# Kernel tuning notes

Hardware: AMD Instinct MI355X
Metric: run time of the kernel (lower is better)

## Reference

```python
import jax, jax.numpy as jnp
import numpy as np

N_NODES = 50000
N_EDGES = 640000
D = 128


def setup_inputs() -> dict:
    key = jax.random.key(0)
    k1, k2, k3, k4, k5 = jax.random.split(key, 5)
    graph_embedding = jax.random.normal(k1, (N_NODES, D), dtype=jnp.float32)
    # xavier_uniform for a (1, D) tensor: bound = sqrt(6/(1+D))
    bound = float(np.sqrt(6.0 / (1 + D)))
    weight = jax.random.uniform(k2, (1, D), dtype=jnp.float32, minval=-bound, maxval=bound)
    e_feat = jax.random.randint(k3, (N_EDGES,), 0, 31, dtype=jnp.int64)
    src = jax.random.randint(k4, (N_EDGES,), 0, N_NODES, dtype=jnp.int64)
    dst = jax.random.randint(k5, (N_EDGES,), 0, N_NODES, dtype=jnp.int64)
    return {"graph_embedding": graph_embedding, "weight": weight,
            "e_feat": e_feat, "src": src, "dst": dst}


def reference(graph_embedding, weight, e_feat, src, dst):
    n_nodes = graph_embedding.shape[0]
    # emb == ft == ft0 == ft1 == ft2 == ft3 in the original module
    emb = jax.nn.elu(graph_embedding * weight)  # [N, D]
    e = e_feat.reshape(-1, 1).astype(jnp.float32)  # [E, 1] (module casts to float)
    # res + sum_k where(e==type_k, ft_k, 0) with all ft_k identical ->
    # per-edge multiplier 1 + matched-type indicators
    mult = (1.0
            + (e == 0.0).astype(emb.dtype)
            + (e == 6.0).astype(emb.dtype)
            + (e == 14.0).astype(emb.dtype)
            + (e == 30.0).astype(emb.dtype))  # [E, 1]
    msgs = emb[src] * mult  # [E, D] gather + mask-select
    # fn.sum('m','ft'): scatter-add messages to destination nodes
    return jax.ops.segment_sum(msgs, dst, num_segments=n_nodes)  # [N, D]
```

## Files before the change

### kernel.cpp

```cpp
#include <hip/hip_runtime.h>

#define D        128
#define NT       256
#define NBMAX    256
#define CAPB     8192
#define KA_BLKS  320
#define OVF_CAP  65536

typedef __attribute__((ext_vector_type(4))) _Float16 half4;
typedef __attribute__((ext_vector_type(4))) float    f32x4;

__device__ __forceinline__ float4 elu_mul(float4 g, float4 w) {
    float4 v;
    v.x = g.x * w.x; v.y = g.y * w.y; v.z = g.z * w.z; v.w = g.w * w.w;
    v.x = (v.x > 0.0f) ? v.x : (__expf(v.x) - 1.0f);
    v.y = (v.y > 0.0f) ? v.y : (__expf(v.y) - 1.0f);
    v.z = (v.z > 0.0f) ? v.z : (__expf(v.z) - 1.0f);
    v.w = (v.w > 0.0f) ? v.w : (__expf(v.w) - 1.0f);
    return v;
}

__global__ __launch_bounds__(NT)
void emb_kernel(const float* __restrict__ ge, const float* __restrict__ weight,
                _Float16* __restrict__ emb, int* __restrict__ cursor,
                int* __restrict__ ovf_cnt, int n_nodes, int nbins) {
    int t = blockIdx.x * NT + threadIdx.x;
    if (t < nbins) cursor[t] = t * CAPB;
    if (t == 0) *ovf_cnt = 0;

    int quads = n_nodes * (D / 4);
    if (t < quads) {
        int col = (t & 31) * 4;
        float4 g = *reinterpret_cast<const float4*>(ge + (size_t)t * 4);
        float4 w = *reinterpret_cast<const float4*>(weight + col);
        float4 v = elu_mul(g, w);
        half4 h;
        h.x = (_Float16)v.x; h.y = (_Float16)v.y;
        h.z = (_Float16)v.z; h.w = (_Float16)v.w;
        *reinterpret_cast<half4*>(emb + (size_t)t * 4) = h;
    }
}

__global__ __launch_bounds__(NT)
void bin_kernel(const int* __restrict__ e_feat, const int* __restrict__ src,
                const int* __restrict__ dst, int* __restrict__ cursor,
                uint2* __restrict__ binned, int* __restrict__ ovf_cnt,
                uint2* __restrict__ ovf, int n_edges, int nbins, int per_block) {
    __shared__ int hist[NBMAX];
    __shared__ int base[NBMAX];
    __shared__ int rk[NBMAX];
    int t = threadIdx.x;
    for (int i = t; i < NBMAX; i += NT) { hist[i] = 0; rk[i] = 0; }
    __syncthreads();

    int e0 = blockIdx.x * per_block;
    int e1 = e0 + per_block; if (e1 > n_edges) e1 = n_edges;

    for (int e = e0 + t; e < e1; e += NT)
        atomicAdd(&hist[dst[e] >> 8], 1);
    __syncthreads();

    for (int b = t; b < nbins; b += NT)
        base[b] = hist[b] ? atomicAdd(&cursor[b], hist[b]) : 0;
    __syncthreads();

    for (int e = e0 + t; e < e1; e += NT) {
        int d = dst[e];
        int b = d >> 8;
        int f = e_feat[e];
        unsigned int flag = (f == 0 || f == 6 || f == 14 || f == 30) ? 1u : 0u;
        unsigned int rec  = (unsigned int)src[e] | (flag << 31);
        int r = atomicAdd(&rk[b], 1);
        long long pos = (long long)base[b] + r;
        if (pos < (long long)(b + 1) * CAPB) {
            binned[pos] = make_uint2(rec, (unsigned int)(d & 255));
        } else {
            int op = atomicAdd(ovf_cnt, 1);
            if (op < OVF_CAP) ovf[op] = make_uint2(rec, (unsigned int)d);
        }
    }
}

__global__ __launch_bounds__(1024)
void csr_kernel(const uint2* __restrict__ binned, const int* __restrict__ cursor,
                int* __restrict__ offsets, unsigned int* __restrict__ bucket,
                int n_nodes, int nbins) {
    __shared__ int s[NBMAX];
    __shared__ int cnt2[NBMAX];
    __shared__ int off2[NBMAX];
    __shared__ int rk2[NBMAX];
    int t = threadIdx.x;
    int b = blockIdx.x;

    int c = 0;
    if (t < nbins) {
        int raw = cursor[t] - t * CAPB;
        c = raw < CAPB ? raw : CAPB;
    }
    if (t < NBMAX) s[t] = c;
    __syncthreads();
    for (int d = 1; d < NBMAX; d <<= 1) {
        int x = 0;
        if (t < NBMAX && t >= d) x = s[t - d];
        __syncthreads();
        if (t < NBMAX) s[t] += x;
        __syncthreads();
    }
    int rawb = cursor[b] - b * CAPB;
    int cntb = rawb < CAPB ? rawb : CAPB;
    int G = s[b] - cntb;
    int total = s[nbins - 1];

    for (int i = t; i < NBMAX; i += 1024) { cnt2[i] = 0; rk2[i] = 0; }
    __syncthreads();
    const uint2* rb = binned + (long long)b * CAPB;
    for (int i = t; i < cntb; i += 1024)
        atomicAdd(&cnt2[rb[i].y], 1);
    __syncthreads();
    if (t < NBMAX) off2[t] = cnt2[t];
    __syncthreads();
    for (int d = 1; d < NBMAX; d <<= 1) {
        int x = 0;
        if (t < NBMAX && t >= d) x = off2[t - d];
        __syncthreads();
        if (t < NBMAX) off2[t] += x;
        __syncthreads();
    }

    int base_node = b << 8;
    if (t < NBMAX) {
        int node = base_node + t;
        if (node <= n_nodes) offsets[node] = G + off2[t] - cnt2[t];
    }
    if (b == nbins - 1 && t == 0) offsets[n_nodes] = total;
    __syncthreads();

    for (int i = t; i < cntb; i += 1024) {
        uint2 r = rb[i];
        int l = (int)r.y;
        int p = atomicAdd(&rk2[l], 1);
        bucket[G + (off2[l] - cnt2[l]) + p] = r.x;
    }
}

__global__ __launch_bounds__(NT)
void gather_kernel(const _Float16* __restrict__ emb,
                   const int* __restrict__ offsets,
                   const unsigned int* __restrict__ bucket,
                   const int* __restrict__ ovf_cnt, const uint2* __restrict__ ovf,
                   float* __restrict__ out, int n_nodes) {
    int tid = blockIdx.x * NT + threadIdx.x;
    int node = tid >> 5;
    if (node >= n_nodes) return;
    int col = (tid & 31) * 4;

    int beg = offsets[node];
    int end = offsets[node + 1];
    float4 acc = make_float4(0.f, 0.f, 0.f, 0.f);

    int i = beg;
    for (; i + 8 <= end; i += 8) {
        unsigned int r0 = bucket[i+0], r1 = bucket[i+1], r2 = bucket[i+2], r3 = bucket[i+3];
        unsigned int r4 = bucket[i+4], r5 = bucket[i+5], r6 = bucket[i+6], r7 = bucket[i+7];
        half4 h0 = *reinterpret_cast<const half4*>(emb + (size_t)(r0 & 0x7FFFFFFFu) * D + col);
        half4 h1 = *reinterpret_cast<const half4*>(emb + (size_t)(r1 & 0x7FFFFFFFu) * D + col);
        half4 h2 = *reinterpret_cast<const half4*>(emb + (size_t)(r2 & 0x7FFFFFFFu) * D + col);
        half4 h3 = *reinterpret_cast<const half4*>(emb + (size_t)(r3 & 0x7FFFFFFFu) * D + col);
        half4 h4 = *reinterpret_cast<const half4*>(emb + (size_t)(r4 & 0x7FFFFFFFu) * D + col);
        half4 h5 = *reinterpret_cast<const half4*>(emb + (size_t)(r5 & 0x7FFFFFFFu) * D + col);
        half4 h6 = *reinterpret_cast<const half4*>(emb + (size_t)(r6 & 0x7FFFFFFFu) * D + col);
        half4 h7 = *reinterpret_cast<const half4*>(emb + (size_t)(r7 & 0x7FFFFFFFu) * D + col);
        float m0 = (r0 >> 31) ? 2.f : 1.f, m1 = (r1 >> 31) ? 2.f : 1.f;
        float m2 = (r2 >> 31) ? 2.f : 1.f, m3 = (r3 >> 31) ? 2.f : 1.f;
        float m4 = (r4 >> 31) ? 2.f : 1.f, m5 = (r5 >> 31) ? 2.f : 1.f;
        float m6 = (r6 >> 31) ? 2.f : 1.f, m7 = (r7 >> 31) ? 2.f : 1.f;
        acc.x += (float)h0.x*m0 + (float)h1.x*m1 + (float)h2.x*m2 + (float)h3.x*m3
               + (float)h4.x*m4 + (float)h5.x*m5 + (float)h6.x*m6 + (float)h7.x*m7;
        acc.y += (float)h0.y*m0 + (float)h1.y*m1 + (float)h2.y*m2 + (float)h3.y*m3
               + (float)h4.y*m4 + (float)h5.y*m5 + (float)h6.y*m6 + (float)h7.y*m7;
        acc.z += (float)h0.z*m0 + (float)h1.z*m1 + (float)h2.z*m2 + (float)h3.z*m3
               + (float)h4.z*m4 + (float)h5.z*m5 + (float)h6.z*m6 + (float)h7.z*m7;
        acc.w += (float)h0.w*m0 + (float)h1.w*m1 + (float)h2.w*m2 + (float)h3.w*m3
               + (float)h4.w*m4 + (float)h5.w*m5 + (float)h6.w*m6 + (float)h7.w*m7;
    }
    for (; i + 4 <= end; i += 4) {
        unsigned int r0 = bucket[i+0], r1 = bucket[i+1], r2 = bucket[i+2], r3 = bucket[i+3];
        half4 h0 = *reinterpret_cast<const half4*>(emb + (size_t)(r0 & 0x7FFFFFFFu) * D + col);
        half4 h1 = *reinterpret_cast<const half4*>(emb + (size_t)(r1 & 0x7FFFFFFFu) * D + col);
        half4 h2 = *reinterpret_cast<const half4*>(emb + (size_t)(r2 & 0x7FFFFFFFu) * D + col);
        half4 h3 = *reinterpret_cast<const half4*>(emb + (size_t)(r3 & 0x7FFFFFFFu) * D + col);
        float m0 = (r0 >> 31) ? 2.f : 1.f, m1 = (r1 >> 31) ? 2.f : 1.f;
        float m2 = (r2 >> 31) ? 2.f : 1.f, m3 = (r3 >> 31) ? 2.f : 1.f;
        acc.x += (float)h0.x*m0 + (float)h1.x*m1 + (float)h2.x*m2 + (float)h3.x*m3;
        acc.y += (float)h0.y*m0 + (float)h1.y*m1 + (float)h2.y*m2 + (float)h3.y*m3;
        acc.z += (float)h0.z*m0 + (float)h1.z*m1 + (float)h2.z*m2 + (float)h3.z*m3;
        acc.w += (float)h0.w*m0 + (float)h1.w*m1 + (float)h2.w*m2 + (float)h3.w*m3;
    }
    for (; i < end; ++i) {
        unsigned int r = bucket[i];
        half4 h = *reinterpret_cast<const half4*>(emb + (size_t)(r & 0x7FFFFFFFu) * D + col);
        float m = (r >> 31) ? 2.f : 1.f;
        acc.x += (float)h.x*m; acc.y += (float)h.y*m;
        acc.z += (float)h.z*m; acc.w += (float)h.w*m;
    }

    int no = *ovf_cnt;
    if (no > 0) {
        if (no > OVF_CAP) no = OVF_CAP;
        for (int k = 0; k < no; ++k) {
            uint2 o = ovf[k];
            if ((int)o.y == node) {
                half4 h = *reinterpret_cast<const half4*>(emb + (size_t)(o.x & 0x7FFFFFFFu) * D + col);
                float m = (o.x >> 31) ? 2.f : 1.f;
                acc.x += (float)h.x*m; acc.y += (float)h.y*m;
                acc.z += (float)h.z*m; acc.w += (float)h.w*m;
            }
        }
    }

    f32x4 o;
    o.x = acc.x; o.y = acc.y; o.z = acc.z; o.w = acc.w;
    __builtin_nontemporal_store(o, reinterpret_cast<f32x4*>(out + (size_t)node * D + col));
}

__global__ void edge_scatter_fallback(const float* __restrict__ ge,
                                      const float* __restrict__ weight,
                                      const int* __restrict__ e_feat,
                                      const int* __restrict__ src,
                                      const int* __restrict__ dst,
                                      float* __restrict__ out, int n_edges) {
    long long tid = (long long)blockIdx.x * blockDim.x + threadIdx.x;
    int edge = (int)(tid >> 5);
    if (edge >= n_edges) return;
    int col = (int)(tid & 31) * 4;
    int e = e_feat[edge];
    float mult = (e == 0 || e == 6 || e == 14 || e == 30) ? 2.0f : 1.0f;
    float4 w = *reinterpret_cast<const float4*>(weight + col);
    float4 g = *reinterpret_cast<const float4*>(ge + (long long)src[edge] * D + col);
    float4 v = elu_mul(g, w);
    float* o = out + (long long)dst[edge] * D + col;
    atomicAdd(o + 0, v.x * mult);
    atomicAdd(o + 1, v.y * mult);
    atomicAdd(o + 2, v.z * mult);
    atomicAdd(o + 3, v.w * mult);
}

extern "C" void kernel_launch(void* const* d_in, const int* in_sizes, int n_in,
                              void* d_out, int out_size, void* d_ws, size_t ws_size,
                              hipStream_t stream) {
    const float* ge     = (const float*)d_in[0];
    const float* weight = (const float*)d_in[1];
    const int*   e_feat = (const int*)d_in[2];
    const int*   src    = (const int*)d_in[3];
    const int*   dst    = (const int*)d_in[4];
    float* out = (float*)d_out;

    int n_edges = in_sizes[2];
    int n_nodes = out_size / D;
    int nbins   = (n_nodes + 255) >> 8;

    auto align256 = [](size_t x) { return (x + 255) & ~(size_t)255; };
    size_t o_emb    = 0;
    size_t o_cursor = o_emb    + align256((size_t)n_nodes * D * sizeof(_Float16));
    size_t o_ovfcnt = o_cursor + align256((size_t)NBMAX * 4);
    size_t o_offs   = o_ovfcnt + 256;
    size_t o_binned = o_offs   + align256((size_t)(n_nodes + 1) * 4);
    size_t o_bucket = o_binned + align256((size_t)NBMAX * CAPB * 8);
    size_t o_ovf    = o_bucket + align256((size_t)n_edges * 4);
    size_t need     = o_ovf + (size_t)OVF_CAP * 8 + 256;

    bool ok = (nbins <= NBMAX) && ((long long)n_edges <= (long long)nbins * CAPB);

    if (ws_size < need || !ok) {
        (void)hipMemsetAsync(d_out, 0, (size_t)out_size * sizeof(float), stream);
        long long total = (long long)n_edges * 32;
        edge_scatter_fallback<<<(int)((total + 255) / 256), 256, 0, stream>>>(
            ge, weight, e_feat, src, dst, out, n_edges);
        return;
    }

    char* ws = (char*)d_ws;
    _Float16*     emb     = (_Float16*)(ws + o_emb);
    int*          cursor  = (int*)(ws + o_cursor);
    int*          ovf_cnt = (int*)(ws + o_ovfcnt);
    int*          offsets = (int*)(ws + o_offs);
    uint2*        binned  = (uint2*)(ws + o_binned);
    unsigned int* bucket  = (unsigned int*)(ws + o_bucket);
    uint2*        ovf     = (uint2*)(ws + o_ovf);

    int quads = n_nodes * (D / 4);
    int k1b = (quads + NT - 1) / NT;
    int per_block = (n_edges + KA_BLKS - 1) / KA_BLKS;

    emb_kernel<<<k1b, NT, 0, stream>>>(ge, weight, emb, cursor, ovf_cnt,
                                       n_nodes, nbins);
    bin_kernel<<<KA_BLKS, NT, 0, stream>>>(e_feat, src, dst, cursor, binned,
                                           ovf_cnt, ovf, n_edges, nbins, per_block);
    csr_kernel<<<nbins, 1024, 0, stream>>>(binned, cursor, offsets, bucket,
                                           n_nodes, nbins);

    long long total = (long long)n_nodes * 32;
    gather_kernel<<<(int)((total + 255) / 256), NT, 0, stream>>>(
        emb, offsets, bucket, ovf_cnt, ovf, out, n_nodes);
}
```

Before: 63.54 us.

## Fuse binning with embedding and use per-block bin cells instead of global cursors

The embedding ELU/fp16 conversion and edge binning now run in one launch, with blocks split between the two roles. Binning writes into fixed per-(block,bin) cells of 64 entries, so the global histogram pass and the atomic cursor reservation are gone. The CSR kernel reads each bin's cells from all 320 blocks with one thread per cell. It writes (offset, degree) pairs into fixed-stride bucket regions, so no global prefix scan is needed. The cost is serial per-thread cell loops in csr_kernel, a larger workspace, and a spill path for cells that overflow.

```diff
diff --git a/kernel.cpp b/kernel.cpp
--- a/kernel.cpp
+++ b/kernel.cpp
@@ -1,11 +1,10 @@
 #include <hip/hip_runtime.h>
 
-#define D        128
-#define NT       256
-#define NBMAX    256
-#define CAPB     8192
-#define KA_BLKS  320
-#define OVF_CAP  65536
+#define D      128
+#define NT     256
+#define KB     320
+#define CAPBB  64
+#define NBMAX  256
 
 typedef __attribute__((ext_vector_type(4))) _Float16 half4;
 typedef __attribute__((ext_vector_type(4))) float    f32x4;
@@ -21,141 +20,137 @@
 }
 
 __global__ __launch_bounds__(NT)
-void emb_kernel(const float* __restrict__ ge, const float* __restrict__ weight,
-                _Float16* __restrict__ emb, int* __restrict__ cursor,
-                int* __restrict__ ovf_cnt, int n_nodes, int nbins) {
-    int t = blockIdx.x * NT + threadIdx.x;
-    if (t < nbins) cursor[t] = t * CAPB;
-    if (t == 0) *ovf_cnt = 0;
-
-    int quads = n_nodes * (D / 4);
-    if (t < quads) {
-        int col = (t & 31) * 4;
-        float4 g = *reinterpret_cast<const float4*>(ge + (size_t)t * 4);
-        float4 w = *reinterpret_cast<const float4*>(weight + col);
-        float4 v = elu_mul(g, w);
-        half4 h;
-        h.x = (_Float16)v.x; h.y = (_Float16)v.y;
-        h.z = (_Float16)v.z; h.w = (_Float16)v.w;
-        *reinterpret_cast<half4*>(emb + (size_t)t * 4) = h;
-    }
-}
-
-__global__ __launch_bounds__(NT)
-void bin_kernel(const int* __restrict__ e_feat, const int* __restrict__ src,
-                const int* __restrict__ dst, int* __restrict__ cursor,
-                uint2* __restrict__ binned, int* __restrict__ ovf_cnt,
-                uint2* __restrict__ ovf, int n_edges, int nbins, int per_block) {
-    __shared__ int hist[NBMAX];
-    __shared__ int base[NBMAX];
-    __shared__ int rk[NBMAX];
-    int t = threadIdx.x;
-    for (int i = t; i < NBMAX; i += NT) { hist[i] = 0; rk[i] = 0; }
-    __syncthreads();
-
-    int e0 = blockIdx.x * per_block;
-    int e1 = e0 + per_block; if (e1 > n_edges) e1 = n_edges;
-
-    for (int e = e0 + t; e < e1; e += NT)
-        atomicAdd(&hist[dst[e] >> 8], 1);
-    __syncthreads();
-
-    for (int b = t; b < nbins; b += NT)
-        base[b] = hist[b] ? atomicAdd(&cursor[b], hist[b]) : 0;
-    __syncthreads();
-
-    for (int e = e0 + t; e < e1; e += NT) {
-        int d = dst[e];
-        int b = d >> 8;
-        int f = e_feat[e];
-        unsigned int flag = (f == 0 || f == 6 || f == 14 || f == 30) ? 1u : 0u;
-        unsigned int rec  = (unsigned int)src[e] | (flag << 31);
-        int r = atomicAdd(&rk[b], 1);
-        long long pos = (long long)base[b] + r;
-        if (pos < (long long)(b + 1) * CAPB) {
-            binned[pos] = make_uint2(rec, (unsigned int)(d & 255));
-        } else {
-            int op = atomicAdd(ovf_cnt, 1);
-            if (op < OVF_CAP) ovf[op] = make_uint2(rec, (unsigned int)d);
+void fused_kernel(const float* __restrict__ ge, const float* __restrict__ weight,
+                  const int* __restrict__ e_feat, const int* __restrict__ src,
+                  const int* __restrict__ dst,
+                  _Float16* __restrict__ emb, uint2* __restrict__ binned,
+                  int* __restrict__ cnts, uint2* __restrict__ spill,
+                  int* __restrict__ spill_cnt,
+                  int n_nodes, int n_edges, int nbins, int per_block) {
+    if ((int)blockIdx.x < KB) {
+        __shared__ int rk[NBMAX];
+        __shared__ int sp;
+        int t = threadIdx.x;
+        for (int i = t; i < NBMAX; i += NT) rk[i] = 0;
+        if (t == 0) sp = 0;
+        __syncthreads();
+
+        int blk = blockIdx.x;
+        int e0 = blk * per_block;
+        int e1 = e0 + per_block; if (e1 > n_edges) e1 = n_edges;
+        for (int e = e0 + t; e < e1; e += NT) {
+            int d = dst[e];
+            int b = d >> 8;
+            int f = e_feat[e];
+            unsigned int flag = (f == 0 || f == 6 || f == 14 || f == 30) ? 1u : 0u;
+            unsigned int rec  = (unsigned int)src[e] | (flag << 31);
+            int r = atomicAdd(&rk[b], 1);
+            if (r < CAPBB) {
+                binned[((size_t)blk * nbins + b) * CAPBB + r] =
+                    make_uint2(rec, (unsigned int)(d & 255));
+            } else {
+                int s = atomicAdd(&sp, 1);
+                spill[(size_t)blk * per_block + s] = make_uint2(rec, (unsigned int)d);
+            }
         }
+        __syncthreads();
+        for (int b = t; b < nbins; b += NT)
+            cnts[blk * nbins + b] = rk[b] < CAPBB ? rk[b] : CAPBB;
+        if (t == 0) spill_cnt[blk] = sp;
+    } else {
+        int t = ((int)blockIdx.x - KB) * NT + threadIdx.x;
+        int quads = n_nodes * (D / 4);
+        if (t < quads) {
+            int col = (t & 31) * 4;
+            float4 g = *reinterpret_cast<const float4*>(ge + (size_t)t * 4);
+            float4 w = *reinterpret_cast<const float4*>(weight + col);
+            float4 v = elu_mul(g, w);
+            half4 h;
+            h.x = (_Float16)v.x; h.y = (_Float16)v.y;
+            h.z = (_Float16)v.z; h.w = (_Float16)v.w;
+            *reinterpret_cast<half4*>(emb + (size_t)t * 4) = h;
+        }
     }
 }
 
 __global__ __launch_bounds__(1024)
-void csr_kernel(const uint2* __restrict__ binned, const int* __restrict__ cursor,
-                int* __restrict__ offsets, unsigned int* __restrict__ bucket,
-                int n_nodes, int nbins) {
-    __shared__ int s[NBMAX];
+void csr_kernel(const uint2* __restrict__ binned, const int* __restrict__ cnts,
+                uint2* __restrict__ offdeg, unsigned int* __restrict__ bucket,
+                const int* __restrict__ spill_cnt, int* __restrict__ spill_total,
+                int n_nodes, int nbins, int capb_out) {
     __shared__ int cnt2[NBMAX];
     __shared__ int off2[NBMAX];
     __shared__ int rk2[NBMAX];
+    __shared__ int cellc[KB];
+    __shared__ int stot;
     int t = threadIdx.x;
     int b = blockIdx.x;
 
-    int c = 0;
-    if (t < nbins) {
-        int raw = cursor[t] - t * CAPB;
-        c = raw < CAPB ? raw : CAPB;
-    }
-    if (t < NBMAX) s[t] = c;
+    for (int i = t; i < NBMAX; i += 1024) { cnt2[i] = 0; rk2[i] = 0; }
+    if (t < KB) cellc[t] = cnts[t * nbins + b];
+    if (t == 0) stot = 0;
     __syncthreads();
-    for (int d = 1; d < NBMAX; d <<= 1) {
-        int x = 0;
-        if (t < NBMAX && t >= d) x = s[t - d];
-        __syncthreads();
-        if (t < NBMAX) s[t] += x;
-        __syncthreads();
-    }
-    int rawb = cursor[b] - b * CAPB;
-    int cntb = rawb < CAPB ? rawb : CAPB;
-    int G = s[b] - cntb;
-    int total = s[nbins - 1];
-
-    for (int i = t; i < NBMAX; i += 1024) { cnt2[i] = 0; rk2[i] = 0; }
+
+    if (t < KB) {
+        const uint2* cell = binned + ((size_t)t * nbins + b) * CAPBB;
+        int c = cellc[t];
+        for (int j = 0; j < c; ++j) atomicAdd(&cnt2[cell[j].y], 1);
+    }
     __syncthreads();
-    const uint2* rb = binned + (long long)b * CAPB;
-    for (int i = t; i < cntb; i += 1024)
-        atomicAdd(&cnt2[rb[i].y], 1);
-    __syncthreads();
+
     if (t < NBMAX) off2[t] = cnt2[t];
     __syncthreads();
-    for (int d = 1; d < NBMAX; d <<= 1) {
+    for (int d2 = 1; d2 < NBMAX; d2 <<= 1) {
         int x = 0;
-        if (t < NBMAX && t >= d) x = off2[t - d];
+        if (t < NBMAX && t >= d2) x = off2[t - d2];
         __syncthreads();
         if (t < NBMAX) off2[t] += x;
         __syncthreads();
     }
 
-    int base_node = b << 8;
+    int G = b * capb_out;
     if (t < NBMAX) {
-        int node = base_node + t;
-        if (node <= n_nodes) offsets[node] = G + off2[t] - cnt2[t];
-    }
-    if (b == nbins - 1 && t == 0) offsets[n_nodes] = total;
+        int node = (b << 8) + t;
+        if (node < n_nodes)
+            offdeg[node] = make_uint2((unsigned int)(G + off2[t] - cnt2[t]),
+                                      (unsigned int)cnt2[t]);
+    }
     __syncthreads();
 
-    for (int i = t; i < cntb; i += 1024) {
-        uint2 r = rb[i];
-        int l = (int)r.y;
-        int p = atomicAdd(&rk2[l], 1);
-        bucket[G + (off2[l] - cnt2[l]) + p] = r.x;
+    if (t < KB) {
+        const uint2* cell = binned + ((size_t)t * nbins + b) * CAPBB;
+        int c = cellc[t];
+        for (int j = 0; j < c; ++j) {
+            uint2 r = cell[j];
+            int l = (int)r.y;
+            int p = atomicAdd(&rk2[l], 1);
+            bucket[G + (off2[l] - cnt2[l]) + p] = r.x;
+        }
+    }
+
+    if (b == 0) {
+        if (t < KB && spill_cnt[t] > 0) atomicAdd(&stot, spill_cnt[t]);
+        __syncthreads();
+        if (t == 0) *spill_total = stot;
     }
 }
 
 __global__ __launch_bounds__(NT)
 void gather_kernel(const _Float16* __restrict__ emb,
-                   const int* __restrict__ offsets,
+                   const uint2* __restrict__ offdeg,
                    const unsigned int* __restrict__ bucket,
-                   const int* __restrict__ ovf_cnt, const uint2* __restrict__ ovf,
-                   float* __restrict__ out, int n_nodes) {
+                   const int* __restrict__ spill_total,
+                   const int* __restrict__ spill_cnt,
+                   const uint2* __restrict__ spill,
+                   float* __restrict__ out, int n_nodes, int per_block) {
     int tid = blockIdx.x * NT + threadIdx.x;
     int node = tid >> 5;
     if (node >= n_nodes) return;
     int col = (tid & 31) * 4;
 
-    int beg = offsets[node];
-    int end = offsets[node + 1];
+    uint2 od = offdeg[node];
+    int beg = (int)od.x;
+    int end = beg + (int)od.y;
     float4 acc = make_float4(0.f, 0.f, 0.f, 0.f);
 
     int i = beg;
@@ -204,16 +199,17 @@
         acc.z += (float)h.z*m; acc.w += (float)h.w*m;
     }
 
-    int no = *ovf_cnt;
-    if (no > 0) {
-        if (no > OVF_CAP) no = OVF_CAP;
-        for (int k = 0; k < no; ++k) {
-            uint2 o = ovf[k];
-            if ((int)o.y == node) {
-                half4 h = *reinterpret_cast<const half4*>(emb + (size_t)(o.x & 0x7FFFFFFFu) * D + col);
-                float m = (o.x >> 31) ? 2.f : 1.f;
-                acc.x += (float)h.x*m; acc.y += (float)h.y*m;
-                acc.z += (float)h.z*m; acc.w += (float)h.w*m;
+    if (*spill_total > 0) {
+        for (int blk = 0; blk < KB; ++blk) {
+            int sc = spill_cnt[blk];
+            for (int j = 0; j < sc; ++j) {
+                uint2 o = spill[(size_t)blk * per_block + j];
+                if ((int)o.y == node) {
+                    half4 h = *reinterpret_cast<const half4*>(emb + (size_t)(o.x & 0x7FFFFFFFu) * D + col);
+                    float m = (o.x >> 31) ? 2.f : 1.f;
+                    acc.x += (float)h.x*m; acc.y += (float)h.y*m;
+                    acc.z += (float)h.z*m; acc.w += (float)h.w*m;
+                }
             }
         }
     }
@@ -258,20 +254,21 @@
     int n_edges = in_sizes[2];
     int n_nodes = out_size / D;
     int nbins   = (n_nodes + 255) >> 8;
+    int per_block = (n_edges + KB - 1) / KB;
+    int capb_out  = KB * CAPBB;
 
     auto align256 = [](size_t x) { return (x + 255) & ~(size_t)255; };
     size_t o_emb    = 0;
-    size_t o_cursor = o_emb    + align256((size_t)n_nodes * D * sizeof(_Float16));
-    size_t o_ovfcnt = o_cursor + align256((size_t)NBMAX * 4);
-    size_t o_offs   = o_ovfcnt + 256;
-    size_t o_binned = o_offs   + align256((size_t)(n_nodes + 1) * 4);
-    size_t o_bucket = o_binned + align256((size_t)NBMAX * CAPB * 8);
-    size_t o_ovf    = o_bucket + align256((size_t)n_edges * 4);
-    size_t need     = o_ovf + (size_t)OVF_CAP * 8 + 256;
-
-    bool ok = (nbins <= NBMAX) && ((long long)n_edges <= (long long)nbins * CAPB);
-
-    if (ws_size < need || !ok) {
+    size_t o_binned = o_emb    + align256((size_t)n_nodes * D * sizeof(_Float16));
+    size_t o_spill  = o_binned + align256((size_t)KB * nbins * CAPBB * 8);
+    size_t o_cnts   = o_spill  + align256((size_t)KB * per_block * 8);
+    size_t o_scnt   = o_cnts   + align256((size_t)KB * nbins * 4);
+    size_t o_stot   = o_scnt   + align256((size_t)KB * 4);
+    size_t o_offdeg = o_stot   + 256;
+    size_t o_bucket = o_offdeg + align256((size_t)n_nodes * 8);
+    size_t need     = o_bucket + align256((size_t)nbins * capb_out * 4);
+
+    if (ws_size < need || nbins > NBMAX) {
         (void)hipMemsetAsync(d_out, 0, (size_t)out_size * sizeof(float), stream);
         long long total = (long long)n_edges * 32;
         edge_scatter_fallback<<<(int)((total + 255) / 256), 256, 0, stream>>>(
@@ -281,25 +278,24 @@
 
     char* ws = (char*)d_ws;
     _Float16*     emb     = (_Float16*)(ws + o_emb);
-    int*          cursor  = (int*)(ws + o_cursor);
-    int*          ovf_cnt = (int*)(ws + o_ovfcnt);
-    int*          offsets = (int*)(ws + o_offs);
     uint2*        binned  = (uint2*)(ws + o_binned);
+    uint2*        spill   = (uint2*)(ws + o_spill);
+    int*          cnts    = (int*)(ws + o_cnts);
+    int*          scnt    = (int*)(ws + o_scnt);
+    int*          stot    = (int*)(ws + o_stot);
+    uint2*        offdeg  = (uint2*)(ws + o_offdeg);
     unsigned int* bucket  = (unsigned int*)(ws + o_bucket);
-    uint2*        ovf     = (uint2*)(ws + o_ovf);
 
     int quads = n_nodes * (D / 4);
-    int k1b = (quads + NT - 1) / NT;
-    int per_block = (n_edges + KA_BLKS - 1) / KA_BLKS;
-
-    emb_kernel<<<k1b, NT, 0, stream>>>(ge, weight, emb, cursor, ovf_cnt,
-                                       n_nodes, nbins);
-    bin_kernel<<<KA_BLKS, NT, 0, stream>>>(e_feat, src, dst, cursor, binned,
-                                           ovf_cnt, ovf, n_edges, nbins, per_block);
-    csr_kernel<<<nbins, 1024, 0, stream>>>(binned, cursor, offsets, bucket,
-                                           n_nodes, nbins);
+    int embBlocks = (quads + NT - 1) / NT;
+
+    fused_kernel<<<KB + embBlocks, NT, 0, stream>>>(
+        ge, weight, e_feat, src, dst, emb, binned, cnts, spill, scnt,
+        n_nodes, n_edges, nbins, per_block);
+    csr_kernel<<<nbins, 1024, 0, stream>>>(binned, cnts, offdeg, bucket,
+                                           scnt, stot, n_nodes, nbins, capb_out);
 
     long long total = (long long)n_nodes * 32;
     gather_kernel<<<(int)((total + 255) / 256), NT, 0, stream>>>(
-        emb, offsets, bucket, ovf_cnt, ovf, out, n_nodes);
-}
+        emb, offdeg, bucket, stot, scnt, spill, out, n_nodes, per_block);
+}
```

After: 57.13 us (median of 2 runs). -10.1%, faster.
